# Kernel tuning notes

Measured on AMD Instinct MI355X. Metric: run time of the kernel, lower is better.

Reference implementation:

```python
import jax, jax.numpy as jnp
import numpy as np
from jax import lax

PAD = 2
M1 = M2 = 12

def _gelu(v):
    return jax.nn.gelu(v, approximate=False)

def _spectral_conv(h, w1, w2):
    # h: [B,C,H,W] real; w1,w2: [C,C,M1,M2] complex64
    B, C, H, W = h.shape
    Wf = W // 2 + 1
    hft = jnp.fft.rfft2(h)  # [B,C,H,Wf] complex
    top = jnp.einsum('bixy,ioxy->boxy', hft[:, :, :M1, :M2], w1)
    bot = jnp.einsum('bixy,ioxy->boxy', hft[:, :, -M1:, :M2], w2)
    out_ft = jnp.zeros((B, C, H, Wf), jnp.complex64)
    out_ft = out_ft.at[:, :, :M1, :M2].set(top)
    out_ft = out_ft.at[:, :, -M1:, :M2].set(bot)
    return jnp.fft.irfft2(out_ft, s=(H, W))

def reference(x, grid, sentence_embeddings, fc0_w, fc0_b, sc_w1, sc_w2, wc_w, wc_b,
              pe1_w, pe1_b, pe2_w, pe2_b,
              sp_w1, sp_b1, sp_w2, sp_b2, sp_w3, sp_b3,
              xp_w1, xp_b1, xp_w2, xp_b2, xp_w3, xp_b3,
              pu_w1, pu_b1, pu_w2, pu_b2, pu_w3, pu_b3,
              fc1_w, fc1_b, fc2_w, fc2_b):
    B = x.shape[0]
    # sentence projection: Linear-ReLU-Linear-ReLU-Linear
    s = jax.nn.relu(sentence_embeddings @ sp_w1 + sp_b1)
    s = jax.nn.relu(s @ sp_w2 + sp_b2)
    sentence_emb = s @ sp_w3 + sp_b3  # [B,16]

    h = jnp.concatenate([x, grid], axis=-1) @ fc0_w + fc0_b  # [B,32,32,C]
    h = h.transpose(0, 3, 1, 2)  # [B,C,32,32]
    h = jnp.pad(h, ((0, 0), (0, 0), (0, PAD), (0, PAD)))  # [B,C,34,34]

    for i in range(4):
        w1 = sc_w1[i, ..., 0] + 1j * sc_w1[i, ..., 1]
        w2 = sc_w2[i, ..., 0] + 1j * sc_w2[i, ..., 1]
        x1 = _spectral_conv(h, w1, w2)
        x2 = jnp.einsum('bchw,oc->bohw', h, wc_w[i]) + wc_b[i][None, :, None, None]
        h = x1 + x2
        if i < 3:
            h = _gelu(h)  # dropout = identity (eval mode)

    # PatchEmbed: conv(k=8,s=4) -> gelu -> 1x1 conv
    p = lax.conv_general_dilated(h, pe1_w, (4, 4), 'VALID',
                                 dimension_numbers=('NCHW', 'OIHW', 'NCHW'))
    p = _gelu(p + pe1_b[None, :, None, None])  # [B,1,7,7]
    p = jnp.einsum('bchw,oc->bohw', p, pe2_w) + pe2_b[None, :, None, None]
    p = p.reshape(B, -1)  # [B,49]

    e = jax.nn.silu(p @ xp_w1 + xp_b1)
    e = jax.nn.silu(e @ xp_w2 + xp_b2)
    x_emb = e @ xp_w3 + xp_b3  # [B,16]

    emb = jnp.concatenate([x_emb, sentence_emb], axis=-1)  # [B,32]
    emb = jax.nn.silu(emb @ pu_w1 + pu_b1)
    emb = jax.nn.silu(emb @ pu_w2 + pu_b2)
    emb = (emb @ pu_w3 + pu_b3).reshape(B, 1, 34, 34)

    h = jnp.concatenate([h, emb], axis=1)  # [B,C+1,34,34]
    h = h[..., :-PAD, :-PAD]  # [B,C+1,32,32]
    h = h.transpose(0, 2, 3, 1)
    h = _gelu(h @ fc1_w + fc1_b)
    out = h @ fc2_w + fc2_b
    return out[..., None, :]  # [B,32,32,1,num_channels]

def setup_inputs() -> dict:
    key = jax.random.key(0)
    ks = iter(jax.random.split(key, 64))
    def rn(shape, scale=1.0):
        return jax.random.normal(next(ks), shape, jnp.float32) * scale
    C = 64
    inp = {
        'x': rn((256, 32, 32, 40)),
        'grid': jax.random.uniform(next(ks), (256, 32, 32, 2), jnp.float32),
        'sentence_embeddings': rn((256, 384)),
        'fc0_w': rn((42, C), 42 ** -0.5), 'fc0_b': jnp.zeros((C,), jnp.float32),
        'sc_w1': rn((4, C, C, M1, M2, 2), 1.0 / (C * C)),
        'sc_w2': rn((4, C, C, M1, M2, 2), 1.0 / (C * C)),
        'wc_w': rn((4, C, C), C ** -0.5), 'wc_b': jnp.zeros((4, C), jnp.float32),
        'pe1_w': rn((1, C, 8, 8), (C * 64) ** -0.5), 'pe1_b': jnp.zeros((1,), jnp.float32),
        'pe2_w': rn((1, 1)), 'pe2_b': jnp.zeros((1,), jnp.float32),
        'sp_w1': rn((384, 32), 384 ** -0.5), 'sp_b1': jnp.zeros((32,), jnp.float32),
        'sp_w2': rn((32, 32), 32 ** -0.5), 'sp_b2': jnp.zeros((32,), jnp.float32),
        'sp_w3': rn((32, 16), 32 ** -0.5), 'sp_b3': jnp.zeros((16,), jnp.float32),
        'xp_w1': rn((49, 32), 49 ** -0.5), 'xp_b1': jnp.zeros((32,), jnp.float32),
        'xp_w2': rn((32, 32), 32 ** -0.5), 'xp_b2': jnp.zeros((32,), jnp.float32),
        'xp_w3': rn((32, 16), 32 ** -0.5), 'xp_b3': jnp.zeros((16,), jnp.float32),
        'pu_w1': rn((32, 128), 32 ** -0.5), 'pu_b1': jnp.zeros((128,), jnp.float32),
        'pu_w2': rn((128, 256), 128 ** -0.5), 'pu_b2': jnp.zeros((256,), jnp.float32),
        'pu_w3': rn((256, 1156), 256 ** -0.5), 'pu_b3': jnp.zeros((1156,), jnp.float32),
        'fc1_w': rn((C + 1, 128), (C + 1) ** -0.5), 'fc1_b': jnp.zeros((128,), jnp.float32),
        'fc2_w': rn((128, 4), 128 ** -0.5), 'fc2_b': jnp.zeros((4,), jnp.float32),
    }
    return inp
```

## Files before the change

### kernel.cpp

```cpp
#include <hip/hip_runtime.h>
#include <hip/hip_bf16.h>
#include <math.h>

typedef __hip_bfloat16 bf16;
typedef __bf16 bfv8 __attribute__((ext_vector_type(8)));
typedef float fv4 __attribute__((ext_vector_type(4)));

__device__ __forceinline__ float bff(const bf16 x){ return __bfloat162float(x); }
__device__ __forceinline__ float gelu_f(float v){
    return 0.5f * v * (1.f + erff(v * 0.70710678118654752f));
}
__device__ __forceinline__ float silu_f(float v){
    return v / (1.f + expf(-v));
}
__device__ __forceinline__ float rdf(const void* p, size_t i, bool f32){
    return f32 ? ((const float*)p)[i] : __bfloat162float(((const bf16*)p)[i]);
}
__device__ __forceinline__ unsigned int packbf2(float a, float b){
    __hip_bfloat162 v;
    v.x = __float2bfloat16(a);
    v.y = __float2bfloat16(b);
    return *reinterpret_cast<unsigned int*>(&v);
}
__device__ __forceinline__ float2 unpackbf2(unsigned int u){
    __hip_bfloat162 v = *reinterpret_cast<__hip_bfloat162*>(&u);
    return make_float2(__bfloat162float(v.x), __bfloat162float(v.y));
}
__device__ __forceinline__ float us2f(unsigned short u){
    unsigned int x = ((unsigned int)u) << 16;
    return __uint_as_float(x);
}
__device__ __forceinline__ unsigned short f2us(float f){
    bf16 v = __float2bfloat16(f);
    return *reinterpret_cast<unsigned short*>(&v);
}


__global__ __launch_bounds__(256) void k_probe(const void* x, float* flag){
    __shared__ int wild;
    int t = threadIdx.x;
    if (t == 0) wild = 0;
    __syncthreads();
    const bf16* xb = (const bf16*)x;
    for (int i = t; i < 1024; i += 256){
        float v = bff(xb[i]);
        if (!(fabsf(v) < 1e10f)) wild = 1;
    }
    __syncthreads();
    if (t == 0) flag[0] = wild ? 1.f : 0.f;
}

__global__ __launch_bounds__(256) void k_tables(float* tabs, float* fwdimg){
    int t = threadIdx.x;
    unsigned int* gBT = (unsigned int*)(tabs + 2448);
    unsigned int* gW2 = (unsigned int*)(tabs + 3536);
    unsigned short* gB1 = (unsigned short*)fwdimg;
    unsigned short* gB2 = (unsigned short*)(fwdimg + 1024);
    const float TWO_PI = 6.283185307179586f;
    for (int i = t; i < 2048; i += 256){
        int row = i >> 6, k = i & 63;
        float v = 0.f;
        if (row < 24 && k < 34){
            int kx = row >> 1, s = row & 1;
            int ph = (kx * k) % 34;
            float ang = TWO_PI * (float)ph / 34.0f;
            float sn, cs;
            sincosf(ang, &sn, &cs);
            v = (s == 0) ? cs : -sn;
        }
        gB1[i] = f2us(v);
    }
    for (int i = t; i < 4608; i += 256){
        int row = i / 96, kk = i - row*96;
        float v = 0.f;
        if (kk < 68){
            int kyi = row >> 1, s = row & 1;
            int y = kk >> 1, p = kk & 1;
            int ky = (kyi < 12) ? kyi : kyi + 10;
            int ph = (ky * y) % 34;
            float ang = TWO_PI * (float)ph / 34.0f;
            float sn, cs;
            sincosf(ang, &sn, &cs);
            float wr = cs, wi = -sn;
            v = (s == 0) ? ((p == 0) ? wr : -wi) : ((p == 0) ? wi : wr);
        }
        gB2[i] = f2us(v);
    }
    for (int i = t; i < 1088; i += 256){
        int n = i >> 4, kd = i & 15;
        int x = n >> 1, ri = n & 1;
        int kx = kd;
        float v0 = 0.f, v1 = 0.f;
        if (kx < 12){
            int ph = (kx * x) % 34;
            float ang = TWO_PI * (float)ph / 34.0f;
            float s, c;
            sincosf(ang, &s, &c);
            float ck = (kx == 0) ? 1.0f : 2.0f;
            float C = ck * c, S = ck * s;
            v0 = (ri == 0) ? C : S;
            v1 = (ri == 0) ? -S : C;
        }
        gBT[i] = packbf2(v0, v1);
    }
    for (int i = t; i < 1088; i += 256){
        int y = i >> 5, kd = i & 31;
        int kyi = kd;
        float v0 = 0.f, v1 = 0.f;
        if (kyi < 24){
            int ky = (kyi < 12) ? kyi : kyi + 10;
            int ph = (ky * y) % 34;
            float ang = TWO_PI * (float)ph / 34.0f;
            float s, c;
            sincosf(ang, &s, &c);
            v0 = c * (1.0f/1156.0f);
            v1 = -s * (1.0f/1156.0f);
        }
        gW2[i] = packbf2(v0, v1);
    }
}

__global__ __launch_bounds__(256) void k_fc0(const void* __restrict__ xin,
                                             const void* __restrict__ grd,
                                             const void* __restrict__ w,
                                             const void* __restrict__ bias,
                                             bf16* __restrict__ h,
                                             const float* __restrict__ flg){
    __shared__ unsigned short sA[256*72];
    __shared__ unsigned short sBT[64*72];
    __shared__ float sb[64];
    const bool f32 = (flg[0] > 0.5f);
    int B = blockIdx.x;
    int b = (B >> 5)*8 + (B & 7);
    int q = (B >> 3) & 3;
    int t = threadIdx.x;
    for (int i = t; i < 4096; i += 256){
        int k = i >> 6, c = i & 63;
        sBT[c*72 + k] = f2us((k < 42) ? rdf(w, (size_t)k*64 + c, f32) : 0.f);
    }
    if (t < 64) sb[t] = rdf(bias, t, f32);
    size_t xbase = ((size_t)b*1024 + q*256)*40;
    for (int i = t; i < 10240; i += 256){
        int p = i / 40, k = i - p*40;
        sA[p*72 + k] = f2us(rdf(xin, xbase + i, f32));
    }
    size_t gbase = ((size_t)b*1024 + q*256)*2;
    for (int i = t; i < 512; i += 256)
        sA[(i >> 1)*72 + 40 + (i & 1)] = f2us(rdf(grd, gbase + i, f32));
    for (int i = t; i < 5632; i += 256){
        int p = i / 22, k = 42 + (i - p*22);
        sA[p*72 + k] = 0;
    }
    __syncthreads();
    int ln = t & 15, qd = (t & 63) >> 4, wv = t >> 6;
    bfv8 bfr[4][2];
    #pragma unroll
    for (int nt = 0; nt < 4; ++nt)
        #pragma unroll
        for (int ks = 0; ks < 2; ++ks)
            bfr[nt][ks] = *reinterpret_cast<const bfv8*>(&sBT[(nt*16 + ln)*72 + ks*32 + qd*8]);
    bfv8 a_[4][2];
    #pragma unroll
    for (int mi = 0; mi < 4; ++mi){
        int mt = wv*4 + mi;
        a_[mi][0] = *reinterpret_cast<const bfv8*>(&sA[(mt*16 + ln)*72 + qd*8]);
        a_[mi][1] = *reinterpret_cast<const bfv8*>(&sA[(mt*16 + ln)*72 + 32 + qd*8]);
    }
    fv4 acc[4][4];
    #pragma unroll
    for (int mi = 0; mi < 4; ++mi)
        #pragma unroll
        for (int nt = 0; nt < 4; ++nt){
            fv4 a = (fv4){0.f,0.f,0.f,0.f};
            a = __builtin_amdgcn_mfma_f32_16x16x32_bf16(a_[mi][0], bfr[nt][0], a, 0, 0, 0);
            a = __builtin_amdgcn_mfma_f32_16x16x32_bf16(a_[mi][1], bfr[nt][1], a, 0, 0, 0);
            acc[mi][nt] = a;
        }
    __syncthreads();
    unsigned int* sCd = (unsigned int*)sA;
    for (int i = t; i < 512; i += 256)
        sCd[(i >> 3)*136 + (i & 7)*17 + 16] = 0;
    #pragma unroll
    for (int mi = 0; mi < 4; ++mi)
        #pragma unroll
        for (int nt = 0; nt < 4; ++nt){
            int c = nt*16 + ln;
            float bb = sb[c];
            int pl = (wv*4 + mi)*16 + qd*4;
            int y = pl >> 5, x = pl & 31;
            int di = c*136 + y*17 + (x >> 1);
            sCd[di]     = packbf2(acc[mi][nt][0] + bb, acc[mi][nt][1] + bb);
            sCd[di + 1] = packbf2(acc[mi][nt][2] + bb, acc[mi][nt][3] + bb);
        }
    __syncthreads();
    unsigned int* hw = (unsigned int*)(h + (size_t)b*73984);
    for (int i = t; i < 8704; i += 256){
        int c = i / 136, d = i - c*136;
        hw[c*578 + q*136 + d] = sCd[i];
    }
    if (q == 3){
        for (int i = t; i < 2176; i += 256){
            int c = i / 34, d = i - c*34;
            hw[c*578 + 544 + d] = 0;
        }
    }
}

__global__ __launch_bounds__(256) void k_fwd(const bf16* __restrict__ h,
                                             unsigned int* __restrict__ hft,
                                             const unsigned short* __restrict__ fwdimg){
    __shared__ unsigned short lds[15360];
    unsigned short* sA1 = lds;
    unsigned short* sA2 = lds + 10368;
    unsigned int* sA1w = (unsigned int*)sA1;
    unsigned int* sA2w = (unsigned int*)sA2;
    const unsigned short* gB1 = fwdimg;
    const unsigned short* gB2 = fwdimg + 2048;
    int blk = blockIdx.x;
    int b = blk >> 4, c0 = (blk & 15) * 4;
    int t = threadIdx.x;
    const unsigned int* srcp = (const unsigned int*)(h + (size_t)b*73984 + (size_t)c0*1156);
    for (int i = t; i < 2312; i += 256){
        int c = i / 578; int rem = i - c*578;
        int y = rem / 17; int d = rem - y*17;
        sA1w[(c*34 + y)*36 + d] = srcp[i];
    }
    for (int i = t; i < 2040; i += 256){
        int r = i / 15, d = i - r*15;
        sA1w[r*36 + 17 + d] = 0;
    }
    for (int i = t; i < 288; i += 256){
        int r = 136 + i / 36, d = i - (i/36)*36;
        sA1w[r*36 + d] = 0;
    }
    for (int i = t; i < 672; i += 256){
        int r = i / 14, d = i - r*14;
        sA2w[r*52 + 34 + d] = 0;
    }
    __syncthreads();
    int ln = t & 15, qd = (t & 63) >> 4, wv = t >> 6;
    {
        int ntw = wv & 1;
        bfv8 b1f[2];
        #pragma unroll
        for (int ks = 0; ks < 2; ++ks)
            b1f[ks] = *reinterpret_cast<const bfv8*>(&gB1[(ntw*16 + ln)*64 + ks*32 + qd*8]);
        int col = ntw*16 + ln;
        int kx = col >> 1, s = col & 1;
        for (int mt = (wv >> 1); mt < 9; mt += 2){
            fv4 acc = (fv4){0.f,0.f,0.f,0.f};
            #pragma unroll
            for (int ks = 0; ks < 2; ++ks){
                bfv8 a = *reinterpret_cast<const bfv8*>(&sA1[(mt*16 + ln)*72 + ks*32 + qd*8]);
                acc = __builtin_amdgcn_mfma_f32_16x16x32_bf16(a, b1f[ks], acc, 0, 0, 0);
            }
            if (col < 24){
                #pragma unroll
                for (int rr = 0; rr < 4; ++rr){
                    int r = mt*16 + qd*4 + rr;
                    if (r < 136){
                        int c = r / 34, y = r - c*34;
                        sA2[(c*12 + kx)*104 + 2*y + s] = f2us(acc[rr]);
                    }
                }
            }
        }
    }
    __syncthreads();
    unsigned short* sC = sA1;
    for (int tau = wv; tau < 9; tau += 4){
        int mt = tau / 3, nt = tau - (tau/3)*3;
        fv4 acc = (fv4){0.f,0.f,0.f,0.f};
        #pragma unroll
        for (int ks = 0; ks < 3; ++ks){
            bfv8 a  = *reinterpret_cast<const bfv8*>(&sA2[(mt*16 + ln)*104 + ks*32 + qd*8]);
            bfv8 bb = *reinterpret_cast<const bfv8*>(&gB2[(nt*16 + ln)*96 + ks*32 + qd*8]);
            acc = __builtin_amdgcn_mfma_f32_16x16x32_bf16(a, bb, acc, 0, 0, 0);
        }
        int col = nt*16 + ln;
        int ky = col >> 1, s = col & 1;
        #pragma unroll
        for (int rr = 0; rr < 4; ++rr){
            int r = mt*16 + qd*4 + rr;
            int c = r / 12, kxx = r - c*12;
            sC[(ky*12 + kxx)*9 + s*4 + c] = f2us(acc[rr]);
        }
    }
    __syncthreads();
    unsigned int* dst = hft + ((size_t)(c0 >> 2)*256 + b)*1152;
    for (int d = t; d < 1152; d += 256){
        int m = d >> 2, j = d & 3;
        unsigned int lo = sC[m*9 + 2*j];
        unsigned int hi = sC[m*9 + 2*j + 1];
        dst[d] = lo | (hi << 16);
    }
}

__global__ __launch_bounds__(256) void k_mixm(const unsigned short* __restrict__ hft,
                                              const void* __restrict__ sc_w1,
                                              const void* __restrict__ sc_w2,
                                              unsigned int* __restrict__ mixed, int layer,
                                              const float* __restrict__ flg){
    __shared__ unsigned short sB[128*136];
    const bool f32 = (flg[0] > 0.5f);
    int B = blockIdx.x;
    int x8 = B & 7, w8 = B >> 3;
    int r4 = w8 & 3, g = w8 >> 2;
    int u = g*8 + x8;
    int mh = u & 1;
    int m  = (u >> 1)*4 + r4;
    int b0 = mh * 128;
    int t = threadIdx.x;
    int kyi = m / 12, kx = m - kyi*12;
    const void* w = (kyi < 12) ? sc_w1 : sc_w2;
    int r = (kyi < 12) ? kyi : kyi - 12;
    size_t wbase = (size_t)layer * 64*64*144*2;
    for (int idx = t; idx < 4096; idx += 256){
        int i = idx >> 6, o = idx & 63;
        size_t off = wbase + (((size_t)idx*12 + r)*12 + kx)*2;
        float wr = rdf(w, off, f32);
        float wi = rdf(w, off+1, f32);
        int kre = ((i >> 2) << 3) + (i & 3);
        sB[o*136 + kre]          = f2us(wr);
        sB[(o+64)*136 + kre]     = f2us(wi);
        sB[o*136 + kre + 4]      = f2us(-wi);
        sB[(o+64)*136 + kre + 4] = f2us(wr);
    }
    __syncthreads();
    int ln = t & 15, qd = (t & 63) >> 4, wv = t >> 6;
    bfv8 af[2][4];
    int arow = b0 + wv*32 + ln;
    #pragma unroll
    for (int tm = 0; tm < 2; ++tm)
        #pragma unroll
        for (int ks = 0; ks < 4; ++ks){
            int gg = ks*4 + qd;
            af[tm][ks] = *reinterpret_cast<const bfv8*>(
                hft + (((size_t)gg*256 + arow + tm*16)*288 + m)*8);
        }
    fv4 acc[2][8];
    #pragma unroll
    for (int tm=0;tm<2;++tm)
        #pragma unroll
        for (int tn=0;tn<8;++tn) acc[tm][tn] = (fv4){0.f,0.f,0.f,0.f};
    #pragma unroll
    for (int ks = 0; ks < 4; ++ks){
        bfv8 bfr[8];
        #pragma unroll
        for (int tn = 0; tn < 8; ++tn)
            bfr[tn] = *reinterpret_cast<const bfv8*>(&sB[(tn*16 + ln)*136 + ks*32 + qd*8]);
        #pragma unroll
        for (int tm = 0; tm < 2; ++tm)
            #pragma unroll
            for (int tn = 0; tn < 8; ++tn)
                acc[tm][tn] = __builtin_amdgcn_mfma_f32_16x16x32_bf16(af[tm][ks], bfr[tn], acc[tm][tn], 0, 0, 0);
    }
    __syncthreads();
    #pragma unroll
    for (int tm = 0; tm < 2; ++tm)
        #pragma unroll
        for (int tn = 0; tn < 8; ++tn)
            #pragma unroll
            for (int rr = 0; rr < 4; ++rr){
                int row = wv*32 + tm*16 + qd*4 + rr;
                int col = tn*16 + ln;
                sB[row*136 + col] = f2us(acc[tm][tn][rr]);
            }
    __syncthreads();
    for (int idx = t; idx < 8192; idx += 256){
        int row = idx >> 6, o = idx & 63;
        unsigned int pr = ((unsigned int)sB[row*136 + o]) |
                          (((unsigned int)sB[row*136 + o + 64]) << 16);
        mixed[((size_t)(b0 + row)*288 + m)*64 + o] = pr;
    }
}

__global__ __launch_bounds__(256) void k_wc(bf16* __restrict__ h,
                                            const void* __restrict__ wc_w,
                                            const void* __restrict__ wc_b,
                                            int layer,
                                            const float* __restrict__ flg){
    __shared__ unsigned short sA[240*72];
    __shared__ unsigned short sBT[64*72];
    __shared__ float sb[64];
    const bool f32 = (flg[0] > 0.5f);
    int blk = blockIdx.x;
    int b = blk & 255, u = blk >> 8;
    int px0 = u*240;
    int npx = 1156 - px0; if (npx > 240) npx = 240;
    int ndp = npx >> 1;
    int t = threadIdx.x;
    size_t wbase = (size_t)layer*4096;
    for (int i = t; i < 4096; i += 256){
        int o = i >> 6, c = i & 63;
        sBT[o*72 + c] = f2us(rdf(wc_w, wbase + i, f32));
    }
    if (t < 64) sb[t] = rdf(wc_b, layer*64 + t, f32);
    const unsigned int* srcd = (const unsigned int*)(h + (size_t)b*73984);
    for (int i = t; i < 7680; i += 256){
        int c = i / 120, dp = i - c*120;
        unsigned int v = (dp < ndp) ? srcd[c*578 + (px0 >> 1) + dp] : 0u;
        sA[(2*dp)*72 + c]     = (unsigned short)(v & 0xffff);
        sA[(2*dp + 1)*72 + c] = (unsigned short)(v >> 16);
    }
    __syncthreads();
    int ln = t & 15, qd = (t & 63) >> 4, wv = t >> 6;
    bfv8 bfr[4][2];
    #pragma unroll
    for (int nt = 0; nt < 4; ++nt)
        #pragma unroll
        for (int ks = 0; ks < 2; ++ks)
            bfr[nt][ks] = *reinterpret_cast<const bfv8*>(&sBT[(nt*16 + ln)*72 + ks*32 + qd*8]);
    bfv8 a_[4][2];
    #pragma unroll
    for (int mi = 0; mi < 4; ++mi){
        int mt = wv + mi*4;
        if (mt < 15){
            a_[mi][0] = *reinterpret_cast<const bfv8*>(&sA[(mt*16 + ln)*72 + qd*8]);
            a_[mi][1] = *reinterpret_cast<const bfv8*>(&sA[(mt*16 + ln)*72 + 32 + qd*8]);
        }
    }
    fv4 acc[4][4];
    #pragma unroll
    for (int mi = 0; mi < 4; ++mi){
        int mt = wv + mi*4;
        if (mt < 15){
            #pragma unroll
            for (int nt = 0; nt < 4; ++nt){
                fv4 a = (fv4){0.f,0.f,0.f,0.f};
                a = __builtin_amdgcn_mfma_f32_16x16x32_bf16(a_[mi][0], bfr[nt][0], a, 0, 0, 0);
                a = __builtin_amdgcn_mfma_f32_16x16x32_bf16(a_[mi][1], bfr[nt][1], a, 0, 0, 0);
                acc[mi][nt] = a;
            }
        }
    }
    __syncthreads();
    unsigned int* sCd = (unsigned int*)sA;
    #pragma unroll
    for (int mi = 0; mi < 4; ++mi){
        int mt = wv + mi*4;
        if (mt < 15){
            #pragma unroll
            for (int nt = 0; nt < 4; ++nt){
                int o = nt*16 + ln;
                float bb = sb[o];
                int p0 = mt*16 + qd*4;
                sCd[o*120 + (p0 >> 1)]     = packbf2(acc[mi][nt][0] + bb, acc[mi][nt][1] + bb);
                sCd[o*120 + (p0 >> 1) + 1] = packbf2(acc[mi][nt][2] + bb, acc[mi][nt][3] + bb);
            }
        }
    }
    __syncthreads();
    unsigned int* dstd = (unsigned int*)(h + (size_t)b*73984);
    for (int i = t; i < 7680; i += 256){
        int o = i / 120, dp = i - o*120;
        if (dp < ndp) dstd[o*578 + (px0 >> 1) + dp] = sCd[o*120 + dp];
    }
}

__global__ __launch_bounds__(256) void k_invm(const unsigned int* __restrict__ mixed,
                                              const float* __restrict__ tabs,
                                              bf16* __restrict__ hio, int layer){
    __shared__ unsigned short lds[18448];
    unsigned short* sA  = lds;
    unsigned short* sG  = lds + 4624;
    unsigned int* ldsw  = (unsigned int*)lds;
    int B = blockIdx.x;
    int x8 = B & 7, s4 = (B >> 3) & 3, z = B >> 5;
    int b  = (z >> 2)*8 + x8;
    int o0 = ((z & 3)*4 + s4)*4;
    int t = threadIdx.x;
    const unsigned short* gBT16 = (const unsigned short*)(tabs + 2448);
    const unsigned short* gW216 = (const unsigned short*)(tabs + 3536);
    const unsigned int* msrc = mixed + (size_t)b*18432 + o0;
    for (int i = t; i < 1152; i += 256){
        int m = i >> 2, ch = i & 3;
        int kyi = m / 12, kx = m - kyi*12;
        ((unsigned int*)sA)[(ch*24 + kyi)*20 + kx] = msrc[(size_t)m*64 + ch];
    }
    for (int i = t; i < 384; i += 256)
        ((unsigned int*)sA)[(i >> 2)*20 + 12 + (i & 3)] = 0;
    for (int i = t; i < 1792; i += 256){
        int r = i >> 5;
        int ch = r / 14, x = 34 + (r - (r/14)*14);
        ((unsigned int*)sG)[(ch*48 + x)*36 + (i & 31)] = 0;
    }
    for (int i = t; i < 1088; i += 256){
        int r = i >> 3;
        int ch = r / 34, x = r - (r/34)*34;
        ((unsigned int*)sG)[(ch*48 + x)*36 + 24 + (i & 7)] = 0;
    }
    __syncthreads();
    int ln = t & 15, qd = (t & 63) >> 4, wv = t >> 6;
    for (int tau = wv; tau < 30; tau += 4){
        int mt = tau / 5, nt = tau - mt*5;
        bfv8 a  = *reinterpret_cast<const bfv8*>(&sA[(mt*16 + ln)*40 + qd*8]);
        bfv8 bb = *reinterpret_cast<const bfv8*>(&gBT16[(nt*16 + ln)*32 + qd*8]);
        fv4 acc = (fv4){0.f,0.f,0.f,0.f};
        acc = __builtin_amdgcn_mfma_f32_16x16x32_bf16(a, bb, acc, 0, 0, 0);
        int col = nt*16 + ln;
        if (col < 68){
            int x = col >> 1, ri = col & 1;
            #pragma unroll
            for (int rr = 0; rr < 4; ++rr){
                int row = mt*16 + qd*4 + rr;
                int ch = row / 24, kyi = row - ch*24;
                sG[(ch*48 + x)*72 + 2*kyi + ri] = f2us(acc[rr]);
            }
        }
    }
    __syncthreads();
    const unsigned int* hsrc = (const unsigned int*)(hio + (size_t)b*73984 + (size_t)o0*1156);
    for (int i = t; i < 2312; i += 256) ldsw[i] = hsrc[i];
    __syncthreads();
    int ch = wv;
    #pragma unroll
    for (int mt = 0; mt < 3; ++mt){
        bfv8 a0 = *reinterpret_cast<const bfv8*>(&gW216[(mt*16 + ln)*64 + qd*8]);
        bfv8 a1 = *reinterpret_cast<const bfv8*>(&gW216[(mt*16 + ln)*64 + 32 + qd*8]);
        #pragma unroll
        for (int nt = 0; nt < 3; ++nt){
            bfv8 b0 = *reinterpret_cast<const bfv8*>(&sG[(ch*48 + nt*16 + ln)*72 + qd*8]);
            bfv8 b1 = *reinterpret_cast<const bfv8*>(&sG[(ch*48 + nt*16 + ln)*72 + 32 + qd*8]);
            fv4 acc = (fv4){0.f,0.f,0.f,0.f};
            acc = __builtin_amdgcn_mfma_f32_16x16x32_bf16(a0, b0, acc, 0, 0, 0);
            acc = __builtin_amdgcn_mfma_f32_16x16x32_bf16(a1, b1, acc, 0, 0, 0);
            int x = nt*16 + ln;
            if (x < 34){
                #pragma unroll
                for (int rr = 0; rr < 4; ++rr){
                    int y = mt*16 + qd*4 + rr;
                    if (y < 34){
                        int off = ch*1156 + y*34 + x;
                        float v = acc[rr] + us2f(lds[off]);
                        if (layer < 3) v = gelu_f(v);
                        lds[off] = f2us(v);
                    }
                }
            }
        }
    }
    __syncthreads();
    unsigned int* hdst = (unsigned int*)(hio + (size_t)b*73984 + (size_t)o0*1156);
    for (int i = t; i < 2312; i += 256) hdst[i] = ldsw[i];
}

__global__ __launch_bounds__(256) void k_pe(const bf16* __restrict__ h,
                                            const void* __restrict__ pw,
                                            const void* __restrict__ pb,
                                            const void* __restrict__ p2w,
                                            const void* __restrict__ p2b,
                                            float* __restrict__ p49,
                                            const float* __restrict__ flg){
    __shared__ float red[256];
    const bool f32 = (flg[0] > 0.5f);
    int bid = blockIdx.x;
    int b = bid / 49, r = bid - b*49;
    int py = r / 7, px = r - py*7;
    int t = threadIdx.x;
    const bf16* hb = h + (size_t)b*73984 + (py*4)*34 + px*4;
    float partial = 0.f;
    for (int tt = t; tt < 4096; tt += 256){
        int c = tt >> 6, k = tt & 63, ky = k >> 3, kx = k & 7;
        partial += bff(hb[(size_t)c*1156 + ky*34 + kx]) * rdf(pw, tt, f32);
    }
    red[t] = partial;
    __syncthreads();
    for (int s = 128; s > 0; s >>= 1){
        if (t < s) red[t] += red[t + s];
        __syncthreads();
    }
    if (t == 0){
        float v = red[0] + rdf(pb, 0, f32);
        v = gelu_f(v);
        p49[bid] = v * rdf(p2w, 0, f32) + rdf(p2b, 0, f32);
    }
}

__global__ __launch_bounds__(64) void k_sent(const void* __restrict__ se,
                                             const void* __restrict__ w1, const void* __restrict__ b1,
                                             const void* __restrict__ w2, const void* __restrict__ b2,
                                             const void* __restrict__ w3, const void* __restrict__ b3,
                                             float* __restrict__ outv,
                                             const float* __restrict__ flg){
    __shared__ float s1[32], s2[32];
    const bool f32 = (flg[0] > 0.5f);
    int b = blockIdx.x, t = threadIdx.x;
    if (t < 32){
        float acc = rdf(b1, t, f32);
        size_t rbase = (size_t)b*384;
        for (int k = 0; k < 384; ++k) acc += rdf(se, rbase + k, f32) * rdf(w1, k*32 + t, f32);
        s1[t] = fmaxf(acc, 0.f);
    }
    __syncthreads();
    if (t < 32){
        float acc = rdf(b2, t, f32);
        for (int k = 0; k < 32; ++k) acc += s1[k] * rdf(w2, k*32 + t, f32);
        s2[t] = fmaxf(acc, 0.f);
    }
    __syncthreads();
    if (t < 16){
        float acc = rdf(b3, t, f32);
        for (int k = 0; k < 32; ++k) acc += s2[k] * rdf(w3, k*16 + t, f32);
        outv[b*16 + t] = acc;
    }
}

__global__ __launch_bounds__(64) void k_xp(const float* __restrict__ p49,
                                           const void* __restrict__ w1, const void* __restrict__ b1,
                                           const void* __restrict__ w2, const void* __restrict__ b2,
                                           const void* __restrict__ w3, const void* __restrict__ b3,
                                           float* __restrict__ outv,
                                           const float* __restrict__ flg){
    __shared__ float s1[32], s2[32];
    const bool f32 = (flg[0] > 0.5f);
    int b = blockIdx.x, t = threadIdx.x;
    if (t < 32){
        float acc = rdf(b1, t, f32);
        const float* row = p49 + b*49;
        for (int k = 0; k < 49; ++k) acc += row[k] * rdf(w1, k*32 + t, f32);
        s1[t] = silu_f(acc);
    }
    __syncthreads();
    if (t < 32){
        float acc = rdf(b2, t, f32);
        for (int k = 0; k < 32; ++k) acc += s1[k] * rdf(w2, k*32 + t, f32);
        s2[t] = silu_f(acc);
    }
    __syncthreads();
    if (t < 16){
        float acc = rdf(b3, t, f32);
        for (int k = 0; k < 32; ++k) acc += s2[k] * rdf(w3, k*16 + t, f32);
        outv[b*16 + t] = acc;
    }
}

__global__ __launch_bounds__(256) void k_puA(const float* __restrict__ xemb,
                                             const float* __restrict__ semb,
                                             const void* __restrict__ w1, const void* __restrict__ b1,
                                             const void* __restrict__ w2, const void* __restrict__ b2,
                                             float* __restrict__ h2buf,
                                             const float* __restrict__ flg){
    __shared__ float ein[32];
    __shared__ float h1[128];
    const bool f32 = (flg[0] > 0.5f);
    int b = blockIdx.x, t = threadIdx.x;
    if (t < 16) ein[t] = xemb[b*16 + t];
    else if (t < 32) ein[t] = semb[b*16 + (t - 16)];
    __syncthreads();
    if (t < 128){
        float acc = rdf(b1, t, f32);
        for (int k = 0; k < 32; ++k) acc += ein[k] * rdf(w1, k*128 + t, f32);
        h1[t] = silu_f(acc);
    }
    __syncthreads();
    {
        float acc = rdf(b2, t, f32);
        for (int k = 0; k < 128; ++k) acc += h1[k] * rdf(w2, k*256 + t, f32);
        h2buf[(size_t)b*256 + t] = silu_f(acc);
    }
}

__global__ __launch_bounds__(256) void k_puB(const float* __restrict__ h2buf,
                                             const void* __restrict__ w3, const void* __restrict__ b3,
                                             float* __restrict__ emb,
                                             const float* __restrict__ flg){
    __shared__ float sh2[256];
    const bool f32 = (flg[0] > 0.5f);
    int blk = blockIdx.x;
    int b = blk & 255, nc = blk >> 8;
    int t = threadIdx.x;
    sh2[t] = h2buf[(size_t)b*256 + t];
    __syncthreads();
    int e = nc*232 + t;
    if (t < 232 && e < 1156){
        float acc = rdf(b3, e, f32);
        if (f32){
            const float* wp = (const float*)w3 + e;
            #pragma unroll 4
            for (int k = 0; k < 256; ++k) acc += sh2[k] * wp[(size_t)k*1156];
        } else {
            const bf16* wp = (const bf16*)w3 + e;
            #pragma unroll 4
            for (int k = 0; k < 256; ++k) acc += sh2[k] * bff(wp[(size_t)k*1156]);
        }
        emb[(size_t)b*1156 + e] = acc;
    }
}

__global__ __launch_bounds__(256, 3) void k_final(const bf16* __restrict__ h,
                                                  const float* __restrict__ emb,
                                                  const void* __restrict__ w1, const void* __restrict__ b1,
                                                  const void* __restrict__ w2, const void* __restrict__ b2,
                                                  void* __restrict__ out,
                                                  const float* __restrict__ flg){
    __shared__ unsigned short sw1t[128*72];
    __shared__ unsigned short sw2t[16*136];
    __shared__ float sw1e[128];
    __shared__ float sb1[128];
    __shared__ float sb2[4];
    __shared__ unsigned short spx[64*66];
    __shared__ float sembp[64];
    __shared__ unsigned short sh2[128*66];
    const bool f32 = (flg[0] > 0.5f);
    int blk = blockIdx.x;
    int b = blk >> 1, half = blk & 1;
    int t = threadIdx.x;
    for (int i = t; i < 8320; i += 256){
        int c = i >> 7, j = i & 127;
        float v = rdf(w1, i, f32);
        if (c < 64) sw1t[j*72 + c] = f2us(v);
        else sw1e[j] = v;
    }
    if (t < 128) sb1[t] = rdf(b1, t, f32);
    for (int i = t; i < 2176; i += 256){
        int n = i / 136, j = i - n*136;
        float v = (n < 4 && j < 128) ? rdf(w2, j*4 + n, f32) : 0.f;
        sw2t[i] = f2us(v);
    }
    if (t < 4) sb2[t] = rdf(b2, t, f32);
    __syncthreads();
    int ln = t & 15, qd = (t & 63) >> 4, wv = t >> 6;
    bfv8 bw1[8][2];
    #pragma unroll
    for (int tn = 0; tn < 8; ++tn)
        #pragma unroll
        for (int ks = 0; ks < 2; ++ks)
            bw1[tn][ks] = *reinterpret_cast<const bfv8*>(&sw1t[(tn*16 + ln)*72 + ks*32 + qd*8]);
    bfv8 bw2[4];
    #pragma unroll
    for (int ks = 0; ks < 4; ++ks)
        bw2[ks] = *reinterpret_cast<const bfv8*>(&sw2t[ln*136 + ks*32 + qd*8]);
    const bf16* hb = h + (size_t)b*73984;
    const float* eb = emb + (size_t)b*1156;
    for (int it = 0; it < 8; ++it){
        int y0 = half*16 + it*2;
        __syncthreads();
        for (int e = t; e < 2048; e += 256){
            int c = e >> 5, d = e & 31;
            int px = d*2;
            int y = y0 + (px >> 5), x = px & 31;
            float v0 = bff(hb[(size_t)c*1156 + y*34 + x]);
            int px1 = px + 1;
            int y1 = y0 + (px1 >> 5), x1 = px1 & 31;
            float v1 = bff(hb[(size_t)c*1156 + y1*34 + x1]);
            ((unsigned int*)spx)[c*33 + d] = packbf2(v0, v1);
        }
        if (t < 64){
            int y = y0 + (t >> 5), x = t & 31;
            sembp[t] = eb[y*34 + x];
        }
        __syncthreads();
        fv4 acc[8];
        #pragma unroll
        for (int tn = 0; tn < 8; ++tn) acc[tn] = (fv4){0.f,0.f,0.f,0.f};
        #pragma unroll
        for (int ks = 0; ks < 2; ++ks){
            union { bfv8 v; unsigned short s[8]; } af;
            #pragma unroll
            for (int j = 0; j < 8; ++j)
                af.s[j] = spx[(ks*32 + qd*8 + j)*66 + wv*16 + ln];
            #pragma unroll
            for (int tn = 0; tn < 8; ++tn)
                acc[tn] = __builtin_amdgcn_mfma_f32_16x16x32_bf16(af.v, bw1[tn][ks], acc[tn], 0, 0, 0);
        }
        float ev[4];
        #pragma unroll
        for (int rr = 0; rr < 4; ++rr) ev[rr] = sembp[wv*16 + qd*4 + rr];
        #pragma unroll
        for (int tn = 0; tn < 8; ++tn){
            int col = tn*16 + ln;
            float we = sw1e[col];
            float bb1 = sb1[col];
            #pragma unroll
            for (int rr = 0; rr < 4; ++rr){
                float v = acc[tn][rr] + ev[rr]*we + bb1;
                sh2[col*66 + wv*16 + qd*4 + rr] = f2us(gelu_f(v));
            }
        }
        __syncthreads();
        fv4 a2 = (fv4){0.f,0.f,0.f,0.f};
        #pragma unroll
        for (int ks = 0; ks < 4; ++ks){
            union { bfv8 v; unsigned short s[8]; } af;
            #pragma unroll
            for (int j = 0; j < 8; ++j)
                af.s[j] = sh2[(ks*32 + qd*8 + j)*66 + wv*16 + ln];
            a2 = __builtin_amdgcn_mfma_f32_16x16x32_bf16(af.v, bw2[ks], a2, 0, 0, 0);
        }
        if (ln < 4){
            float bb2 = sb2[ln];
            #pragma unroll
            for (int rr = 0; rr < 4; ++rr){
                int pxl = wv*16 + qd*4 + rr;
                int y = y0 + (pxl >> 5), x = pxl & 31;
                size_t o = ((size_t)(b*32 + y)*32 + x)*4 + ln;
                float v = a2[rr] + bb2;
                if (f32) ((float*)out)[o] = v;
                else     ((bf16*)out)[o] = __float2bfloat16(v);
            }
        }
    }
}

extern "C" void kernel_launch(void* const* d_in, const int* in_sizes, int n_in,
                              void* d_out, int out_size, void* d_ws, size_t ws_size,
                              hipStream_t stream) {
    (void)in_sizes; (void)n_in; (void)out_size; (void)ws_size;
    const void* x     = d_in[0];
    const void* grd   = d_in[1];
    const void* se    = d_in[2];
    const void* fc0_w = d_in[3];
    const void* fc0_b = d_in[4];
    const void* sc_w1 = d_in[5];
    const void* sc_w2 = d_in[6];
    const void* wc_w  = d_in[7];
    const void* wc_b  = d_in[8];
    const void* pe1_w = d_in[9];
    const void* pe1_b = d_in[10];
    const void* pe2_w = d_in[11];
    const void* pe2_b = d_in[12];
    const void* sp_w1 = d_in[13];
    const void* sp_b1 = d_in[14];
    const void* sp_w2 = d_in[15];
    const void* sp_b2 = d_in[16];
    const void* sp_w3 = d_in[17];
    const void* sp_b3 = d_in[18];
    const void* xp_w1 = d_in[19];
    const void* xp_b1 = d_in[20];
    const void* xp_w2 = d_in[21];
    const void* xp_b2 = d_in[22];
    const void* xp_w3 = d_in[23];
    const void* xp_b3 = d_in[24];
    const void* pu_w1 = d_in[25];
    const void* pu_b1 = d_in[26];
    const void* pu_w2 = d_in[27];
    const void* pu_b2 = d_in[28];
    const void* pu_w3 = d_in[29];
    const void* pu_b3 = d_in[30];
    const void* fc1_w = d_in[31];
    const void* fc1_b = d_in[32];
    const void* fc2_w = d_in[33];
    const void* fc2_b = d_in[34];

    float* ws    = (float*)d_ws;
    bf16*  hA    = (bf16*)ws;
    unsigned int* hft   = (unsigned int*)(ws + 9469952);
    unsigned int* mixed = (unsigned int*)(ws + 14188544);
    float* tabs  = ws + 18907136;
    float* p49   = ws + 18912032;
    float* semb  = ws + 18924576;
    float* xemb  = ws + 18928672;
    float* emb   = ws + 18932768;
    float* flag  = ws + 19228704;
    float* h2buf = (float*)hft;
    float* fwdimg = emb;

    k_probe<<<1, 256, 0, stream>>>(x, flag);
    k_tables<<<1, 256, 0, stream>>>(tabs, fwdimg);
    k_fc0<<<1024, 256, 0, stream>>>(x, grd, fc0_w, fc0_b, hA, flag);

    for (int l = 0; l < 4; ++l){
        k_fwd<<<4096, 256, 0, stream>>>(hA, hft, (const unsigned short*)fwdimg);
        k_mixm<<<576, 256, 0, stream>>>((const unsigned short*)hft, sc_w1, sc_w2, mixed, l, flag);
        k_wc <<<1280, 256, 0, stream>>>(hA, wc_w, wc_b, l, flag);
        k_invm<<<4096, 256, 0, stream>>>(mixed, tabs, hA, l);
    }

    k_pe  <<<256*49, 256, 0, stream>>>(hA, pe1_w, pe1_b, pe2_w, pe2_b, p49, flag);
    k_sent<<<256, 64, 0, stream>>>(se, sp_w1, sp_b1, sp_w2, sp_b2, sp_w3, sp_b3, semb, flag);
    k_xp  <<<256, 64, 0, stream>>>(p49, xp_w1, xp_b1, xp_w2, xp_b2, xp_w3, xp_b3, xemb, flag);
    k_puA <<<256, 256, 0, stream>>>(xemb, semb, pu_w1, pu_b1, pu_w2, pu_b2, h2buf, flag);
    k_puB <<<1280, 256, 0, stream>>>(h2buf, pu_w3, pu_b3, emb, flag);
    k_final<<<512, 256, 0, stream>>>(hA, emb, fc1_w, fc1_b, fc2_w, fc2_b, d_out, flag);
}
```

Measured before the change: 1.165 ms.

## Precompute fc0 weight image once and halve fc0 tile with packed loads

Moves the fc0 weight transpose and bias conversion into the one-time table kernel, so each fc0 block reads a prepacked bf16 weight image straight from global memory into registers instead of rebuilding it in LDS. The fc0 kernel now handles 128 pixels per block (2048 blocks), which shrinks LDS use and raises parallelism. In the bf16 case it copies input rows as 32-bit words without per-element conversion. The trade-off is extra global reads of the weight image per block and more blocks, each with its own fixed overhead.

```diff
diff --git a/kernel.cpp b/kernel.cpp
--- a/kernel.cpp
+++ b/kernel.cpp
@@ -50,13 +50,25 @@
     if (t == 0) flag[0] = wild ? 1.f : 0.f;
 }
 
-__global__ __launch_bounds__(256) void k_tables(float* tabs, float* fwdimg){
-    int t = threadIdx.x;
+__global__ __launch_bounds__(256) void k_tables(float* tabs, float* fwdimg,
+                                                const void* __restrict__ fc0w,
+                                                const void* __restrict__ fc0b,
+                                                const float* __restrict__ flg){
+    int t = threadIdx.x;
+    const bool f32 = (flg[0] > 0.5f);
     unsigned int* gBT = (unsigned int*)(tabs + 2448);
     unsigned int* gW2 = (unsigned int*)(tabs + 3536);
     unsigned short* gB1 = (unsigned short*)fwdimg;
     unsigned short* gB2 = (unsigned short*)(fwdimg + 1024);
+    unsigned short* gF  = (unsigned short*)(fwdimg + 3328);
+    float* gFb = fwdimg + 5632;
     const float TWO_PI = 6.283185307179586f;
+    for (int i = t; i < 4608; i += 256){
+        int c = i / 72, k = i - c*72;
+        float v = (k < 42) ? rdf(fc0w, (size_t)k*64 + c, f32) : 0.f;
+        gF[i] = f2us(v);
+    }
+    if (t < 64) gFb[t] = rdf(fc0b, t, f32);
     for (int i = t; i < 2048; i += 256){
         int row = i >> 6, k = i & 63;
         float v = 0.f;
@@ -122,53 +134,60 @@
 
 __global__ __launch_bounds__(256) void k_fc0(const void* __restrict__ xin,
                                              const void* __restrict__ grd,
-                                             const void* __restrict__ w,
-                                             const void* __restrict__ bias,
+                                             const unsigned short* __restrict__ img,
                                              bf16* __restrict__ h,
                                              const float* __restrict__ flg){
-    __shared__ unsigned short sA[256*72];
-    __shared__ unsigned short sBT[64*72];
-    __shared__ float sb[64];
+    __shared__ unsigned short sA[128*72];
     const bool f32 = (flg[0] > 0.5f);
     int B = blockIdx.x;
-    int b = (B >> 5)*8 + (B & 7);
-    int q = (B >> 3) & 3;
-    int t = threadIdx.x;
-    for (int i = t; i < 4096; i += 256){
-        int k = i >> 6, c = i & 63;
-        sBT[c*72 + k] = f2us((k < 42) ? rdf(w, (size_t)k*64 + c, f32) : 0.f);
-    }
-    if (t < 64) sb[t] = rdf(bias, t, f32);
-    size_t xbase = ((size_t)b*1024 + q*256)*40;
-    for (int i = t; i < 10240; i += 256){
-        int p = i / 40, k = i - p*40;
-        sA[p*72 + k] = f2us(rdf(xin, xbase + i, f32));
-    }
-    size_t gbase = ((size_t)b*1024 + q*256)*2;
-    for (int i = t; i < 512; i += 256)
-        sA[(i >> 1)*72 + 40 + (i & 1)] = f2us(rdf(grd, gbase + i, f32));
-    for (int i = t; i < 5632; i += 256){
-        int p = i / 22, k = 42 + (i - p*22);
-        sA[p*72 + k] = 0;
+    int b = (B >> 6)*8 + (B & 7);
+    int u = (B >> 3) & 7;
+    int t = threadIdx.x;
+    unsigned int* sAw = (unsigned int*)sA;
+    if (!f32){
+        const unsigned int* xd = (const unsigned int*)xin;
+        size_t base = ((size_t)b*1024 + u*128)*20;
+        for (int i = t; i < 2560; i += 256){
+            int p = i / 20, kd = i - p*20;
+            sAw[p*36 + kd] = xd[base + i];
+        }
+        const unsigned int* gd = (const unsigned int*)grd;
+        size_t gb = (size_t)b*1024 + (size_t)u*128;
+        if (t < 128) sAw[t*36 + 20] = gd[gb + t];
+    } else {
+        const float* xf = (const float*)xin;
+        size_t base = ((size_t)b*1024 + u*128)*40;
+        for (int i = t; i < 2560; i += 256){
+            int p = i / 20, kd = i - p*20;
+            sAw[p*36 + kd] = packbf2(xf[base + 2*i], xf[base + 2*i + 1]);
+        }
+        const float* gf = (const float*)grd;
+        size_t gb = ((size_t)b*1024 + u*128)*2;
+        if (t < 128) sAw[t*36 + 20] = packbf2(gf[gb + 2*t], gf[gb + 2*t + 1]);
+    }
+    for (int i = t; i < 1920; i += 256){
+        int p = i / 15, j = i - p*15;
+        sAw[p*36 + 21 + j] = 0;
     }
     __syncthreads();
     int ln = t & 15, qd = (t & 63) >> 4, wv = t >> 6;
+    const float* gbias = (const float*)(img + 4608);
     bfv8 bfr[4][2];
     #pragma unroll
     for (int nt = 0; nt < 4; ++nt)
         #pragma unroll
         for (int ks = 0; ks < 2; ++ks)
-            bfr[nt][ks] = *reinterpret_cast<const bfv8*>(&sBT[(nt*16 + ln)*72 + ks*32 + qd*8]);
-    bfv8 a_[4][2];
-    #pragma unroll
-    for (int mi = 0; mi < 4; ++mi){
-        int mt = wv*4 + mi;
+            bfr[nt][ks] = *reinterpret_cast<const bfv8*>(&img[(nt*16 + ln)*72 + ks*32 + qd*8]);
+    bfv8 a_[2][2];
+    #pragma unroll
+    for (int mi = 0; mi < 2; ++mi){
+        int mt = wv*2 + mi;
         a_[mi][0] = *reinterpret_cast<const bfv8*>(&sA[(mt*16 + ln)*72 + qd*8]);
         a_[mi][1] = *reinterpret_cast<const bfv8*>(&sA[(mt*16 + ln)*72 + 32 + qd*8]);
     }
-    fv4 acc[4][4];
-    #pragma unroll
-    for (int mi = 0; mi < 4; ++mi)
+    fv4 acc[2][4];
+    #pragma unroll
+    for (int mi = 0; mi < 2; ++mi)
         #pragma unroll
         for (int nt = 0; nt < 4; ++nt){
             fv4 a = (fv4){0.f,0.f,0.f,0.f};
@@ -178,27 +197,29 @@
         }
     __syncthreads();
     unsigned int* sCd = (unsigned int*)sA;
-    for (int i = t; i < 512; i += 256)
-        sCd[(i >> 3)*136 + (i & 7)*17 + 16] = 0;
-    #pragma unroll
-    for (int mi = 0; mi < 4; ++mi)
+    {
+        int c = t >> 2, r = t & 3;
+        sCd[c*68 + r*17 + 16] = 0;
+    }
+    #pragma unroll
+    for (int mi = 0; mi < 2; ++mi)
         #pragma unroll
         for (int nt = 0; nt < 4; ++nt){
             int c = nt*16 + ln;
-            float bb = sb[c];
-            int pl = (wv*4 + mi)*16 + qd*4;
+            float bb = gbias[c];
+            int pl = (wv*2 + mi)*16 + qd*4;
             int y = pl >> 5, x = pl & 31;
-            int di = c*136 + y*17 + (x >> 1);
+            int di = c*68 + y*17 + (x >> 1);
             sCd[di]     = packbf2(acc[mi][nt][0] + bb, acc[mi][nt][1] + bb);
             sCd[di + 1] = packbf2(acc[mi][nt][2] + bb, acc[mi][nt][3] + bb);
         }
     __syncthreads();
     unsigned int* hw = (unsigned int*)(h + (size_t)b*73984);
-    for (int i = t; i < 8704; i += 256){
-        int c = i / 136, d = i - c*136;
-        hw[c*578 + q*136 + d] = sCd[i];
-    }
-    if (q == 3){
+    for (int i = t; i < 4352; i += 256){
+        int c = i / 68, d = i - c*68;
+        hw[c*578 + u*68 + d] = sCd[i];
+    }
+    if (u == 7){
         for (int i = t; i < 2176; i += 256){
             int c = i / 34, d = i - c*34;
             hw[c*578 + 544 + d] = 0;
@@ -857,8 +878,8 @@
     float* fwdimg = emb;
 
     k_probe<<<1, 256, 0, stream>>>(x, flag);
-    k_tables<<<1, 256, 0, stream>>>(tabs, fwdimg);
-    k_fc0<<<1024, 256, 0, stream>>>(x, grd, fc0_w, fc0_b, hA, flag);
+    k_tables<<<1, 256, 0, stream>>>(tabs, fwdimg, fc0_w, fc0_b, flag);
+    k_fc0<<<2048, 256, 0, stream>>>(x, grd, (const unsigned short*)(fwdimg + 3328), hA, flag);
 
     for (int l = 0; l < 4; ++l){
         k_fwd<<<4096, 256, 0, stream>>>(hA, hft, (const unsigned short*)fwdimg);
```

New measurement: 1.139 ms. -2.2%, faster.
